# Optimization experiments

Hardware: AMD Instinct MI355X
Metric: run time of the kernel (lower is better)

Reference implementation:

```python
import jax, jax.numpy as jnp
import numpy as np

K = 8
TEMP = 0.05
EPS = 1e-8


def setup_inputs() -> dict:
    key = jax.random.key(0)
    k1, k2, k3, k4, k5, k6 = jax.random.split(key, 6)
    N, D, H = 8192, 1024, 64
    h0 = jax.random.normal(k1, (N, D), dtype=jnp.float32)
    coords = jax.random.uniform(k2, (N, 2), dtype=jnp.float32)
    # tiny MLP params: Linear(2,H) -> ReLU -> Linear(H,1) -> Sigmoid
    W1 = jax.random.normal(k3, (2, H), dtype=jnp.float32) * (1.0 / np.sqrt(2))
    b1 = jnp.zeros((H,), dtype=jnp.float32)
    W2 = jax.random.normal(k4, (H, 1), dtype=jnp.float32) * (1.0 / np.sqrt(H))
    b2 = jnp.zeros((1,), dtype=jnp.float32)
    return {"h0": h0, "coords": coords, "W1": W1, "b1": b1, "W2": W2, "b2": b2}


def reference(h0, coords, W1, b1, W2, b2):
    # pairwise euclidean distances [N, N]
    sq = jnp.sum(coords * coords, axis=-1)                      # [N]
    d2 = sq[:, None] + sq[None, :] - 2.0 * (coords @ coords.T)  # [N, N]
    dist = jnp.sqrt(jnp.maximum(d2, 0.0))

    # k+1 nearest (smallest dist), drop self (index 0)
    _, idx = jax.lax.top_k(-dist, K + 1)                        # [N, K+1]
    knn_idx = idx[:, 1:]                                        # [N, K]

    # gather neighbor features [N, K, D]
    neighbor_feats = h0[knn_idx]

    # cosine similarity between h_i and each neighbor (torch eps semantics)
    num = jnp.einsum('nd,nkd->nk', h0, neighbor_feats)          # [N, K]
    ni = jnp.maximum(jnp.linalg.norm(h0, axis=-1), EPS)         # [N]
    nj = jnp.maximum(jnp.linalg.norm(neighbor_feats, axis=-1), EPS)  # [N, K]
    sim = num / (ni[:, None] * nj)

    # spatial weights from gathered distances
    d_knn = jnp.take_along_axis(dist, knn_idx, axis=1)          # [N, K]
    spatial_w = jnp.exp(-d_knn / TEMP)

    density_input = jnp.stack(
        [sim.mean(axis=1), spatial_w.mean(axis=1)], axis=1)     # [N, 2]

    hmid = jax.nn.relu(density_input @ W1 + b1)
    density = jax.nn.sigmoid(hmid @ W2 + b2)                    # [N, 1]
    return density
```

## Files before the change

kernel.cpp:

```cpp
#include <hip/hip_runtime.h>
#include <math.h>

#define NROWS 8192
#define DIM   1024
#define GRID  64
#define CELLW 0.015625f
#define LPR   16

__device__ __forceinline__ int cell_of(float v) {
    int c = (int)(v * 64.0f);
    return c < 0 ? 0 : (c > 63 ? 63 : c);
}

__device__ __forceinline__ float np_d2(float xi, float yi, float sqi,
                                       float xj, float yj) {
    float sqj = __fadd_rn(__fmul_rn(xj, xj), __fmul_rn(yj, yj));
    float G   = fmaf(yi, yj, __fmul_rn(xi, xj));
    return __fsub_rn(__fadd_rn(sqi, sqj), __fmul_rn(2.0f, G));
}

__global__ __launch_bounds__(1024) void build_grid_kernel(
    const float* __restrict__ coords,
    int* __restrict__ cellStart,
    float4* __restrict__ sxyz) {

    __shared__ int lcnt[4096];
    __shared__ int wsum[16];
    const int t = threadIdx.x;

    for (int i = t; i < 4096; i += 1024) lcnt[i] = 0;
    __syncthreads();

    float2 pc[8]; int pcell[8];
#pragma unroll
    for (int k = 0; k < 8; ++k) {
        int i = t + 1024 * k;
        float2 c = ((const float2*)coords)[i];
        pc[k] = c;
        pcell[k] = cell_of(c.y) * GRID + cell_of(c.x);
        atomicAdd(&lcnt[pcell[k]], 1);
    }
    __syncthreads();

    int c0 = lcnt[t*4+0], c1 = lcnt[t*4+1], c2 = lcnt[t*4+2], c3 = lcnt[t*4+3];
    int s1 = c0, s2 = c0 + c1, s3 = s2 + c2, s4 = s3 + c3;
    int lane = t & 63, wid = t >> 6;
    int inc = s4;
#pragma unroll
    for (int off = 1; off < 64; off <<= 1) {
        int o = __shfl_up(inc, off, 64);
        if (lane >= off) inc += o;
    }
    if (lane == 63) wsum[wid] = inc;
    __syncthreads();
    int wbase = 0;
    for (int w = 0; w < wid; ++w) wbase += wsum[w];
    int excl = wbase + inc - s4;

    cellStart[t*4+0] = excl;
    cellStart[t*4+1] = excl + s1;
    cellStart[t*4+2] = excl + s2;
    cellStart[t*4+3] = excl + s3;
    if (t == 1023) cellStart[4096] = excl + s4;
    lcnt[t*4+0] = excl;
    lcnt[t*4+1] = excl + s1;
    lcnt[t*4+2] = excl + s2;
    lcnt[t*4+3] = excl + s3;
    __syncthreads();

#pragma unroll
    for (int k = 0; k < 8; ++k) {
        int pos = atomicAdd(&lcnt[pcell[k]], 1);
        float x = pc[k].x, y = pc[k].y;
        float sq = __fadd_rn(__fmul_rn(x, x), __fmul_rn(y, y));
        sxyz[pos] = make_float4(x, y, sq, __int_as_float(t + 1024 * k));
    }
}

__global__ __launch_bounds__(256) void knn_kernel(
    const int* __restrict__ cellStart,
    const float4* __restrict__ sxyz,
    unsigned long long* __restrict__ chosen_ws) {

    const int sub = threadIdx.x & (LPR - 1);
    const int g   = (blockIdx.x * 256 + threadIdx.x) / LPR;

    const float4 me = sxyz[g];
    const float xi = me.x, yi = me.y, sqi = me.z;
    const int row = __float_as_int(me.w);
    const int cx = cell_of(xi), cy = cell_of(yi);

    unsigned long long best[10], merged[10];
    int C = 2;
    while (true) {
#pragma unroll
        for (int s = 0; s < 10; ++s) best[s] = ~0ULL;
        int x0 = max(0, cx - C), x1 = min(GRID - 1, cx + C);
        int y0 = max(0, cy - C), y1 = min(GRID - 1, cy + C);
        for (int yy = y0; yy <= y1; ++yy) {
            int s = cellStart[yy * GRID + x0];
            int e = cellStart[yy * GRID + x1 + 1];
            for (int t = s + sub; t < e; t += LPR) {
                float4 c = sxyz[t];
                float d2  = __fsub_rn(__fadd_rn(sqi, c.z),
                                      __fmul_rn(2.0f, fmaf(yi, c.y, __fmul_rn(xi, c.x))));
                float dst = __fsqrt_rn(fmaxf(d2, 0.0f));
                unsigned long long key =
                    ((unsigned long long)__float_as_uint(dst) << 32)
                    | (unsigned int)__float_as_int(c.w);
                if (key < best[9]) {
                    best[9] = key;
#pragma unroll
                    for (int ss = 9; ss >= 1; --ss) {
                        unsigned long long a = best[ss - 1], b = best[ss];
                        unsigned long long lo = a < b ? a : b;
                        unsigned long long hi = a < b ? b : a;
                        best[ss - 1] = lo;
                        best[ss]     = hi;
                    }
                }
            }
        }
#pragma unroll
        for (int r = 0; r < 10; ++r) {
            unsigned long long mn = best[0];
#pragma unroll
            for (int off = 1; off < LPR; off <<= 1) {
                unsigned long long o = __shfl_xor(mn, off, 64);
                mn = (o < mn) ? o : mn;
            }
            if (best[0] == mn) {
#pragma unroll
                for (int ss = 0; ss < 9; ++ss) best[ss] = best[ss + 1];
                best[9] = ~0ULL;
            }
            merged[r] = mn;
        }
        bool done = false;
        if (merged[9] != ~0ULL) {
            float d9 = __uint_as_float((unsigned int)(merged[9] >> 32));
            if (d9 + 1.0e-3f <= (float)C * CELLW) done = true;
        }
        if (done || C >= GRID) break;
        C <<= 1; if (C > GRID) C = GRID;
    }

    if (sub == 0) {
        unsigned long long* o = chosen_ws + (size_t)row * 10;
#pragma unroll
        for (int r = 0; r < 10; ++r) o[r] = merged[r];
    }
}

__global__ __launch_bounds__(256) void gather_kernel(
    const float* __restrict__ h0,
    const unsigned long long* __restrict__ chosen_ws,
    const float4* __restrict__ sxyz,
    float* __restrict__ pdot,
    float* __restrict__ norms) {

    const int widx = threadIdx.x >> 6;
    const int lane = threadIdx.x & 63;
    const int bid  = blockIdx.x;
    const int g    = (bid & 7) * (NROWS / 8) + (bid >> 3);
    const int row  = __float_as_int(sxyz[g].w);

    const float4* hi = (const float4*)(h0 + (size_t)row * DIM);
    float4 a[4];
#pragma unroll
    for (int t = 0; t < 4; ++t) a[t] = hi[lane + 64 * t];

    const unsigned long long* ch = chosen_ws + (size_t)row * 10;

    for (int s = widx; s <= 10; s += 4) {
        float p = 0.f;
        if (s == 10) {
#pragma unroll
            for (int t = 0; t < 4; ++t)
                p += a[t].x * a[t].x + a[t].y * a[t].y + a[t].z * a[t].z + a[t].w * a[t].w;
#pragma unroll
            for (int off = 1; off < 64; off <<= 1) p += __shfl_xor(p, off, 64);
            if (lane == 0) norms[row] = sqrtf(p);
        } else {
            int j = (int)(ch[s] & 0xFFFFFFFFu);
            const float4* hj = (const float4*)(h0 + (size_t)j * DIM);
#pragma unroll
            for (int t = 0; t < 4; ++t) {
                float4 b = hj[lane + 64 * t];
                p += a[t].x * b.x + a[t].y * b.y + a[t].z * b.z + a[t].w * b.w;
            }
#pragma unroll
            for (int off = 1; off < 64; off <<= 1) p += __shfl_xor(p, off, 64);
            if (lane == 0) pdot[(size_t)row * 10 + s] = p;
        }
    }
}

__global__ __launch_bounds__(256) void final_kernel(
    const float* __restrict__ coords,
    const unsigned long long* __restrict__ chosen_ws,
    const float* __restrict__ pdot,
    const float* __restrict__ norms,
    const float* __restrict__ W1, const float* __restrict__ b1,
    const float* __restrict__ W2, const float* __restrict__ b2,
    float* __restrict__ out) {

    const int widx = threadIdx.x >> 6;
    const int lane = threadIdx.x & 63;
    const int row  = blockIdx.x * 4 + widx;

    const float2 ci = ((const float2*)coords)[row];
    const float xi = ci.x, yi = ci.y;
    const float sqi = __fadd_rn(__fmul_rn(xi, xi), __fmul_rn(yi, yi));

    unsigned long long chosen[10];
    const unsigned long long* ch = chosen_ws + (size_t)row * 10;
#pragma unroll
    for (int r = 0; r < 10; ++r) chosen[r] = ch[r];

    auto clamped_d2 = [&](unsigned long long key) -> float {
        int j = (int)(key & 0xFFFFFFFFu);
        float2 cj = ((const float2*)coords)[j];
        return fmaxf(np_d2(xi, yi, sqi, cj.x, cj.y), 0.0f);
    };
    const float m0 = clamped_d2(chosen[0]);
    const float m1 = clamped_d2(chosen[1]);
    const float m2 = clamped_d2(chosen[2]);
    const float m8 = clamped_d2(chosen[8]);
    const float m9 = clamped_d2(chosen[9]);

    const float WIN = 2.0e-6f;
    const bool fpair = (m1 - m0) <= WIN;
    const bool ftri  = fpair && ((m2 - m0) <= WIN);
    const bool f89   = (m9 - m8) <= WIN;

    float wd[3];
    wd[0] = ftri ? (1.f / 3.f) : (fpair ? 0.5f : 1.0f);
    wd[1] = ftri ? (1.f / 3.f) : (fpair ? 0.5f : 0.0f);
    wd[2] = ftri ? (1.f / 3.f) : 0.0f;
    const float wc0 = f89 ? 0.5f : 1.0f;
    const float wc1 = f89 ? 0.5f : 0.0f;

    const float ni = fmaxf(norms[row], 1e-8f);

    float sim[10], sw[10];
#pragma unroll
    for (int r = 0; r < 10; ++r) {
        int   j   = (int)(chosen[r] & 0xFFFFFFFFu);
        float dst = __uint_as_float((unsigned int)(chosen[r] >> 32));
        float nj  = fmaxf(norms[j], 1e-8f);
        sim[r] = pdot[(size_t)row * 10 + r] / (ni * nj);
        sw[r]  = expf(__fdiv_rn(-dst, 0.05f));
    }

    float Ssim = 0.f, Ssw = 0.f;
#pragma unroll
    for (int r = 0; r < 9; ++r) { Ssim += sim[r]; Ssw += sw[r]; }

    const float w1a = W1[lane], w1b = W1[64 + lane];
    const float b1l = b1[lane], w2l = W2[lane], b2s = b2[0];

    float outacc = 0.f;
#pragma unroll
    for (int d = 0; d < 3; ++d) {
#pragma unroll
        for (int c = 0; c < 2; ++c) {
            float wgt = wd[d] * (c ? wc1 : wc0);
            float simsum = Ssim - sim[d] + (c ? (sim[9] - sim[8]) : 0.f);
            float swsum  = Ssw  - sw[d]  + (c ? (sw[9]  - sw[8])  : 0.f);
            float di0 = simsum * 0.125f;
            float di1 = swsum  * 0.125f;
            float hm = fmaxf(di0 * w1a + di1 * w1b + b1l, 0.f);
            float v  = hm * w2l;
#pragma unroll
            for (int off = 1; off < 64; off <<= 1) v += __shfl_xor(v, off, 64);
            float z = v + b2s;
            outacc += wgt * (1.f / (1.f + expf(-z)));
        }
    }

    if (lane == 0) out[row] = outacc;
}

extern "C" void kernel_launch(void* const* d_in, const int* in_sizes, int n_in,
                              void* d_out, int out_size, void* d_ws, size_t ws_size,
                              hipStream_t stream) {
    const float* h0     = (const float*)d_in[0];
    const float* coords = (const float*)d_in[1];
    const float* W1     = (const float*)d_in[2];
    const float* b1     = (const float*)d_in[3];
    const float* W2     = (const float*)d_in[4];
    const float* b2     = (const float*)d_in[5];
    float* out = (float*)d_out;

    char* ws = (char*)d_ws;
    unsigned long long* chosen_ws = (unsigned long long*)(ws);
    float*  pdot      = (float*)(ws + 655360);
    float*  norms     = (float*)(ws + 983040);
    float4* sxyz      = (float4*)(ws + 1015808);
    int*    cellStart = (int*)(ws + 1146880);

    build_grid_kernel<<<1, 1024, 0, stream>>>(coords, cellStart, sxyz);
    knn_kernel       <<<NROWS * LPR / 256, 256, 0, stream>>>(cellStart, sxyz, chosen_ws);
    gather_kernel    <<<NROWS, 256, 0, stream>>>(h0, chosen_ws, sxyz, pdot, norms);
    final_kernel     <<<NROWS / 4, 256, 0, stream>>>(coords, chosen_ws, pdot, norms,
                                                     W1, b1, W2, b2, out);
}
```

Before: 58.98 us.

## Fuse gather and final kernels, recomputing neighbor norms in-block via shared memory

Merges the gather and final kernels into one launch. Each neighbor's squared norm is computed alongside its dot product, and the results are passed through shared memory, so the pdot/norms workspace round-trip and a separate kernel launch go away. The cost is extra FMAs per neighbor row, three idle waves while wave 0 runs the MLP tail, and a __syncthreads per block.

```diff
diff --git a/kernel.cpp b/kernel.cpp
--- a/kernel.cpp
+++ b/kernel.cpp
@@ -152,12 +152,16 @@
     }
 }
 
-__global__ __launch_bounds__(256) void gather_kernel(
+__global__ __launch_bounds__(256) void gather_final_kernel(
     const float* __restrict__ h0,
+    const float* __restrict__ coords,
     const unsigned long long* __restrict__ chosen_ws,
     const float4* __restrict__ sxyz,
-    float* __restrict__ pdot,
-    float* __restrict__ norms) {
+    const float* __restrict__ W1, const float* __restrict__ b1,
+    const float* __restrict__ W2, const float* __restrict__ b2,
+    float* __restrict__ out) {
+
+    __shared__ float2 pq[11];
 
     const int widx = threadIdx.x >> 6;
     const int lane = threadIdx.x & 63;
@@ -173,14 +177,12 @@
     const unsigned long long* ch = chosen_ws + (size_t)row * 10;
 
     for (int s = widx; s <= 10; s += 4) {
-        float p = 0.f;
+        float p = 0.f, q = 0.f;
         if (s == 10) {
 #pragma unroll
             for (int t = 0; t < 4; ++t)
                 p += a[t].x * a[t].x + a[t].y * a[t].y + a[t].z * a[t].z + a[t].w * a[t].w;
-#pragma unroll
-            for (int off = 1; off < 64; off <<= 1) p += __shfl_xor(p, off, 64);
-            if (lane == 0) norms[row] = sqrtf(p);
+            q = p;
         } else {
             int j = (int)(ch[s] & 0xFFFFFFFFu);
             const float4* hj = (const float4*)(h0 + (size_t)j * DIM);
@@ -188,33 +190,25 @@
             for (int t = 0; t < 4; ++t) {
                 float4 b = hj[lane + 64 * t];
                 p += a[t].x * b.x + a[t].y * b.y + a[t].z * b.z + a[t].w * b.w;
-            }
-#pragma unroll
-            for (int off = 1; off < 64; off <<= 1) p += __shfl_xor(p, off, 64);
-            if (lane == 0) pdot[(size_t)row * 10 + s] = p;
-        }
-    }
-}
-
-__global__ __launch_bounds__(256) void final_kernel(
-    const float* __restrict__ coords,
-    const unsigned long long* __restrict__ chosen_ws,
-    const float* __restrict__ pdot,
-    const float* __restrict__ norms,
-    const float* __restrict__ W1, const float* __restrict__ b1,
-    const float* __restrict__ W2, const float* __restrict__ b2,
-    float* __restrict__ out) {
-
-    const int widx = threadIdx.x >> 6;
-    const int lane = threadIdx.x & 63;
-    const int row  = blockIdx.x * 4 + widx;
+                q += b.x * b.x + b.y * b.y + b.z * b.z + b.w * b.w;
+            }
+        }
+#pragma unroll
+        for (int off = 1; off < 64; off <<= 1) {
+            p += __shfl_xor(p, off, 64);
+            q += __shfl_xor(q, off, 64);
+        }
+        if (lane == 0) pq[s] = make_float2(p, q);
+    }
+    __syncthreads();
+
+    if (widx != 0) return;
 
     const float2 ci = ((const float2*)coords)[row];
     const float xi = ci.x, yi = ci.y;
     const float sqi = __fadd_rn(__fmul_rn(xi, xi), __fmul_rn(yi, yi));
 
     unsigned long long chosen[10];
-    const unsigned long long* ch = chosen_ws + (size_t)row * 10;
 #pragma unroll
     for (int r = 0; r < 10; ++r) chosen[r] = ch[r];
 
@@ -241,15 +235,14 @@
     const float wc0 = f89 ? 0.5f : 1.0f;
     const float wc1 = f89 ? 0.5f : 0.0f;
 
-    const float ni = fmaxf(norms[row], 1e-8f);
+    const float ni = fmaxf(sqrtf(pq[10].x), 1e-8f);
 
     float sim[10], sw[10];
 #pragma unroll
     for (int r = 0; r < 10; ++r) {
-        int   j   = (int)(chosen[r] & 0xFFFFFFFFu);
         float dst = __uint_as_float((unsigned int)(chosen[r] >> 32));
-        float nj  = fmaxf(norms[j], 1e-8f);
-        sim[r] = pdot[(size_t)row * 10 + r] / (ni * nj);
+        float nj  = fmaxf(sqrtf(pq[r].y), 1e-8f);
+        sim[r] = pq[r].x / (ni * nj);
         sw[r]  = expf(__fdiv_rn(-dst, 0.05f));
     }
 
@@ -295,14 +288,11 @@
 
     char* ws = (char*)d_ws;
     unsigned long long* chosen_ws = (unsigned long long*)(ws);
-    float*  pdot      = (float*)(ws + 655360);
-    float*  norms     = (float*)(ws + 983040);
     float4* sxyz      = (float4*)(ws + 1015808);
     int*    cellStart = (int*)(ws + 1146880);
 
-    build_grid_kernel<<<1, 1024, 0, stream>>>(coords, cellStart, sxyz);
-    knn_kernel       <<<NROWS * LPR / 256, 256, 0, stream>>>(cellStart, sxyz, chosen_ws);
-    gather_kernel    <<<NROWS, 256, 0, stream>>>(h0, chosen_ws, sxyz, pdot, norms);
-    final_kernel     <<<NROWS / 4, 256, 0, stream>>>(coords, chosen_ws, pdot, norms,
-                                                     W1, b1, W2, b2, out);
-}
+    build_grid_kernel  <<<1, 1024, 0, stream>>>(coords, cellStart, sxyz);
+    knn_kernel         <<<NROWS * LPR / 256, 256, 0, stream>>>(cellStart, sxyz, chosen_ws);
+    gather_final_kernel<<<NROWS, 256, 0, stream>>>(h0, coords, chosen_ws, sxyz,
+                                                   W1, b1, W2, b2, out);
+}
```

New measurement: 63.69 us. 8.0% more time.
